# Optimization experiments

Hardware: AMD Instinct MI355X
Metric: run time of the kernel (lower is better)

Reference implementation:

```python
import jax, jax.numpy as jnp
import numpy as np

B = 16      # number of point clouds
N = 4096    # points per cloud (max segment size, static)
D = 3       # xyz


def setup_inputs() -> dict:
    key = jax.random.key(0)
    k1, k2 = jax.random.split(key)
    pred = jax.random.normal(k1, (B * N, D), dtype=jnp.float32)
    target = jax.random.normal(k2, (B * N, D), dtype=jnp.float32)
    # sorted batch assignment with equal-size segments (so N_max is static)
    batch = jnp.repeat(jnp.arange(B, dtype=jnp.int64), N)
    return {"pred": pred, "target": target, "batch": batch}


def _to_dense_batch(x, batch):
    # Faithful to torch_geometric.utils.to_dense_batch: scatter each point into
    # its (cloud, within-cloud-position) slot; padding slots stay zero.
    T = x.shape[0]
    counts = jax.ops.segment_sum(jnp.ones((T,), jnp.int32), batch, num_segments=B)
    starts = jnp.concatenate([jnp.zeros((1,), jnp.int32), jnp.cumsum(counts)[:-1]])
    pos = jnp.arange(T, dtype=jnp.int32) - starts[batch]
    dense = jnp.zeros((B, N, x.shape[1]), x.dtype).at[batch, pos].set(x)
    return dense


def _chamfer(x, y):
    # pytorch3d.loss.chamfer_distance defaults: squared L2, point_reduction="mean",
    # batch_reduction="mean"; no lengths -> padded zeros count as points (as in source).
    x2 = jnp.sum(x * x, axis=-1)                      # [B, N]
    y2 = jnp.sum(y * y, axis=-1)                      # [B, N]
    xy = jnp.einsum("bid,bjd->bij", x, y)             # [B, N, N]
    d2 = x2[:, :, None] + y2[:, None, :] - 2.0 * xy   # [B, N, N] squared dists
    cham_x = jnp.mean(jnp.min(d2, axis=2), axis=1)    # x -> nearest y, mean over points
    cham_y = jnp.mean(jnp.min(d2, axis=1), axis=1)    # y -> nearest x
    return jnp.mean(cham_x + cham_y)                  # batch mean of summed directions


def reference(pred, target, batch):
    dense_x = _to_dense_batch(pred, batch)
    dense_y = _to_dense_batch(target, batch)
    return _chamfer(dense_x, dense_y)
```

## Files before the change

kernel.cpp:

```cpp
#include <hip/hip_runtime.h>


typedef __attribute__((ext_vector_type(8))) short bf16x8;
typedef __attribute__((ext_vector_type(16))) float floatx16;

#define BB 16
#define NN 4096
#define T  256
#define NPTS (BB * NN)
#define RS 4
#define XC (4 * RS * 32)
#define NXB (NN / XC)
#define YS 2
#define YH (NN / YS)
#define YC 512
#define NC (YH / YC)
#define ONEBF 0x3F80u

__device__ __forceinline__ unsigned int f2bf(float f) {
    unsigned int u = __float_as_uint(f);
    u += 0x7fffu + ((u >> 16) & 1u);
    return u >> 16;
}
__device__ __forceinline__ float bf2f(unsigned int h) {
    return __uint_as_float(h << 16);
}

__global__ __launch_bounds__(T) void chamfer_prep(
    const float* __restrict__ pred, const float* __restrict__ target,
    uint4* __restrict__ rec0, uint4* __restrict__ rec1)
{
    int g = blockIdx.x * T + threadIdx.x;
    int set = g >> 16;
    int idx = g & (NPTS - 1);
    const float* yp = (set ? pred : target) + (size_t)idx * 3;
    float y0 = yp[0], y1 = yp[1], y2 = yp[2];
    unsigned int h0 = f2bf(y0), h1 = f2bf(y1), h2 = f2bf(y2);
    unsigned int H0 = f2bf(-2.f * bf2f(h0));
    unsigned int H1 = f2bf(-2.f * bf2f(h1));
    unsigned int H2 = f2bf(-2.f * bf2f(h2));
    unsigned int L0 = f2bf(-2.f * (y0 - bf2f(h0)));
    unsigned int L1 = f2bf(-2.f * (y1 - bf2f(h1)));
    unsigned int L2 = f2bf(-2.f * (y2 - bf2f(h2)));
    float ysq = fmaf(y0, y0, fmaf(y1, y1, y2 * y2));
    unsigned int sh = f2bf(ysq);
    unsigned int sl = f2bf(ysq - bf2f(sh));
    rec0[g] = make_uint4(H0 | (H1 << 16), H2 | (H0 << 16),
                         H1 | (H2 << 16), L0 | (L1 << 16));
    rec1[g] = make_uint4(L2 | (ONEBF << 16), ONEBF | (sh << 16),
                         sl, 0u);
}

__global__ __launch_bounds__(T, 2) void chamfer_main(
    const float* __restrict__ pred, const float* __restrict__ target,
    const uint4* __restrict__ rec0, const uint4* __restrict__ rec1,
    float* __restrict__ rowp)
{
    __shared__ uint4 ldsy[2][2][YC];

    const int xb  = blockIdx.x;
    const int b   = blockIdx.y;
    const int dir = blockIdx.z >> 1;
    const int ys  = blockIdx.z & 1;
    const float* xsrc = (dir ? target : pred) + (size_t)b * NN * 3;
    const size_t ygbase = (size_t)dir * NPTS + (size_t)b * NN + (size_t)ys * YH;
    const int tid  = threadIdx.x;
    const int lane = tid & 63, w = tid >> 6;
    const int kg   = lane >> 5, m = lane & 31;

    union U { uint4 q; bf16x8 v; };
    U au[RS];
#pragma unroll
    for (int s = 0; s < RS; ++s) {
        int xi = xb * XC + w * (RS * 32) + s * 32 + m;
        const float* xp = xsrc + (size_t)xi * 3;
        float x0 = xp[0], x1 = xp[1], x2 = xp[2];
        unsigned int h0 = f2bf(x0), h1 = f2bf(x1), h2 = f2bf(x2);
        unsigned int L0 = f2bf(x0 - bf2f(h0));
        unsigned int L1 = f2bf(x1 - bf2f(h1));
        unsigned int L2 = f2bf(x2 - bf2f(h2));
        float xsq = fmaf(x0, x0, fmaf(x1, x1, x2 * x2));
        unsigned int sh = f2bf(xsq);
        unsigned int sl = f2bf(xsq - bf2f(sh));
        au[s].q = make_uint4(kg ? (h2 | (sh << 16))    : (h0 | (h1 << 16)),
                             kg ? (sl | (ONEBF << 16)) : (h2 | (L0 << 16)),
                             kg ? ONEBF                : (L1 | (L2 << 16)),
                             kg ? 0u                   : (h0 | (h1 << 16)));
    }

    floatx16 acc[RS], zacc;
#pragma unroll
    for (int r = 0; r < 16; ++r) zacc[r] = 0.f;
#pragma unroll
    for (int s = 0; s < RS; ++s)
#pragma unroll
        for (int r = 0; r < 16; ++r) acc[s][r] = 3.402823466e38f;

    ldsy[0][0][tid]     = rec0[ygbase + tid];
    ldsy[0][0][T + tid] = rec0[ygbase + T + tid];
    ldsy[0][1][tid]     = rec1[ygbase + tid];
    ldsy[0][1][T + tid] = rec1[ygbase + T + tid];
    __syncthreads();

    for (int c = 0; c < NC; ++c) {
        const int cur = c & 1, nxt = cur ^ 1;
        uint4 s0a, s0b, s1a, s1b;
        if (c + 1 < NC) {
            size_t base = ygbase + (size_t)(c + 1) * YC;
            s0a = rec0[base + tid];
            s0b = rec0[base + T + tid];
            s1a = rec1[base + tid];
            s1b = rec1[base + T + tid];
        }
        U b0, b1;
        b0.q = ldsy[cur][kg][m];
        b1.q = ldsy[cur][kg][32 + m];
#pragma unroll 2
        for (int p = 0; p < YC / 64; ++p) {
            U n0, n1;
            int q = (p + 1) & 7;
            n0.q = ldsy[cur][kg][q * 64 + m];
            n1.q = ldsy[cur][kg][q * 64 + 32 + m];
#pragma unroll
            for (int s = 0; s < RS; ++s) {
                floatx16 d0 = __builtin_amdgcn_mfma_f32_32x32x16_bf16(
                    au[s].v, b0.v, zacc, 0, 0, 0);
                floatx16 d1 = __builtin_amdgcn_mfma_f32_32x32x16_bf16(
                    au[s].v, b1.v, zacc, 0, 0, 0);
#pragma unroll
                for (int r = 0; r < 16; ++r)
                    acc[s][r] = fminf(fminf(acc[s][r], d0[r]), d1[r]);
            }
            b0 = n0; b1 = n1;
        }
        if (c + 1 < NC) {
            ldsy[nxt][0][tid]     = s0a;
            ldsy[nxt][0][T + tid] = s0b;
            ldsy[nxt][1][tid]     = s1a;
            ldsy[nxt][1][T + tid] = s1b;
        }
        __syncthreads();
    }

    float* rp = rowp + ((size_t)((dir * BB + b) * YS + ys)) * NN + xb * XC;
#pragma unroll
    for (int s = 0; s < RS; ++s) {
#pragma unroll
        for (int r = 0; r < 16; ++r) {
            float v = acc[s][r];
            v = fminf(v, __shfl_xor(v, 1, 64));
            v = fminf(v, __shfl_xor(v, 2, 64));
            v = fminf(v, __shfl_xor(v, 4, 64));
            v = fminf(v, __shfl_xor(v, 8, 64));
            v = fminf(v, __shfl_xor(v, 16, 64));
            if (m == 0) {
                int row = (r & 3) + 8 * (r >> 2) + 4 * kg;
                rp[w * (RS * 32) + s * 32 + row] = v;
            }
        }
    }
}

__global__ __launch_bounds__(T) void chamfer_final(
    const float* __restrict__ rowp, float* __restrict__ out)
{
    float s = 0.f;
    for (int e = blockIdx.x * T + threadIdx.x; e < 2 * BB * NN;
         e += gridDim.x * T) {
        int g = e >> 12, x = e & (NN - 1);
        float v = fminf(rowp[(size_t)(2 * g) * NN + x],
                        rowp[(size_t)(2 * g + 1) * NN + x]);
        s += fmaxf(v, 0.f);
    }
#pragma unroll
    for (int off = 32; off > 0; off >>= 1)
        s += __shfl_down(s, off, 64);
    __shared__ float wsum[4];
    if ((threadIdx.x & 63) == 0) wsum[threadIdx.x >> 6] = s;
    __syncthreads();
    if (threadIdx.x == 0) {
        float t = wsum[0] + wsum[1] + wsum[2] + wsum[3];
        atomicAdd(out, t * (1.0f / (BB * NN)));
    }
}

extern "C" void kernel_launch(void* const* d_in, const int* in_sizes, int n_in,
                              void* d_out, int out_size, void* d_ws, size_t ws_size,
                              hipStream_t stream) {
    const float* pred   = (const float*)d_in[0];
    const float* target = (const float*)d_in[1];
    float* out  = (float*)d_out;
    uint4* rec0 = (uint4*)d_ws;
    uint4* rec1 = rec0 + 2 * NPTS;
    float* rowp = (float*)(rec1 + 2 * NPTS);

    hipMemsetAsync(out, 0, sizeof(float), stream);
    chamfer_prep<<<2 * NPTS / T, T, 0, stream>>>(pred, target, rec0, rec1);
    dim3 grid(NXB, BB, 2 * YS);
    chamfer_main<<<grid, T, 0, stream>>>(pred, target, rec0, rec1, rowp);
    chamfer_final<<<128, T, 0, stream>>>(rowp, out);
}
```

Measured before the change: 95.74 us.

## Halve per-wave row tiles and drop LDS double buffering for higher occupancy

Reduces rows per wave from 4 to 2 tiles, which doubles the number of x-blocks, and doubles the y chunk size so there are fewer chunk iterations. It replaces the register-staged double-buffered LDS prefetch with a single buffer loaded between two barriers, and requests 4 waves per EU instead of 2. The aim is to lower register pressure and hide latency through more resident waves rather than software pipelining. In exchange, global loads are no longer overlapped with MFMA work inside a block, and each loaded y-tile is reused across fewer x rows.

```diff
diff --git a/kernel.cpp b/kernel.cpp
--- a/kernel.cpp
+++ b/kernel.cpp
@@ -8,12 +8,12 @@
 #define NN 4096
 #define T  256
 #define NPTS (BB * NN)
-#define RS 4
+#define RS 2
 #define XC (4 * RS * 32)
 #define NXB (NN / XC)
 #define YS 2
 #define YH (NN / YS)
-#define YC 512
+#define YC 1024
 #define NC (YH / YC)
 #define ONEBF 0x3F80u
 
@@ -51,12 +51,14 @@
                          sl, 0u);
 }
 
-__global__ __launch_bounds__(T, 2) void chamfer_main(
+__global__ __launch_bounds__(T)
+__attribute__((amdgpu_waves_per_eu(4, 4)))
+void chamfer_main(
     const float* __restrict__ pred, const float* __restrict__ target,
     const uint4* __restrict__ rec0, const uint4* __restrict__ rec1,
     float* __restrict__ rowp)
 {
-    __shared__ uint4 ldsy[2][2][YC];
+    __shared__ uint4 ldsy[2][YC];
 
     const int xb  = blockIdx.x;
     const int b   = blockIdx.y;
@@ -96,50 +98,29 @@
 #pragma unroll
         for (int r = 0; r < 16; ++r) acc[s][r] = 3.402823466e38f;
 
-    ldsy[0][0][tid]     = rec0[ygbase + tid];
-    ldsy[0][0][T + tid] = rec0[ygbase + T + tid];
-    ldsy[0][1][tid]     = rec1[ygbase + tid];
-    ldsy[0][1][T + tid] = rec1[ygbase + T + tid];
-    __syncthreads();
-
     for (int c = 0; c < NC; ++c) {
-        const int cur = c & 1, nxt = cur ^ 1;
-        uint4 s0a, s0b, s1a, s1b;
-        if (c + 1 < NC) {
-            size_t base = ygbase + (size_t)(c + 1) * YC;
-            s0a = rec0[base + tid];
-            s0b = rec0[base + T + tid];
-            s1a = rec1[base + tid];
-            s1b = rec1[base + T + tid];
+        __syncthreads();
+        for (int i = tid; i < YC; i += T) {
+            ldsy[0][i] = rec0[ygbase + c * YC + i];
+            ldsy[1][i] = rec1[ygbase + c * YC + i];
         }
-        U b0, b1;
-        b0.q = ldsy[cur][kg][m];
-        b1.q = ldsy[cur][kg][32 + m];
+        __syncthreads();
 #pragma unroll 2
-        for (int p = 0; p < YC / 64; ++p) {
-            U n0, n1;
-            int q = (p + 1) & 7;
-            n0.q = ldsy[cur][kg][q * 64 + m];
-            n1.q = ldsy[cur][kg][q * 64 + 32 + m];
+        for (int t = 0; t < YC / 32; t += 2) {
+            U bu0, bu1;
+            bu0.q = ldsy[kg][t * 32 + m];
+            bu1.q = ldsy[kg][t * 32 + 32 + m];
 #pragma unroll
             for (int s = 0; s < RS; ++s) {
                 floatx16 d0 = __builtin_amdgcn_mfma_f32_32x32x16_bf16(
-                    au[s].v, b0.v, zacc, 0, 0, 0);
+                    au[s].v, bu0.v, zacc, 0, 0, 0);
                 floatx16 d1 = __builtin_amdgcn_mfma_f32_32x32x16_bf16(
-                    au[s].v, b1.v, zacc, 0, 0, 0);
+                    au[s].v, bu1.v, zacc, 0, 0, 0);
 #pragma unroll
                 for (int r = 0; r < 16; ++r)
                     acc[s][r] = fminf(fminf(acc[s][r], d0[r]), d1[r]);
             }
-            b0 = n0; b1 = n1;
         }
-        if (c + 1 < NC) {
-            ldsy[nxt][0][tid]     = s0a;
-            ldsy[nxt][0][T + tid] = s0b;
-            ldsy[nxt][1][tid]     = s1a;
-            ldsy[nxt][1][T + tid] = s1b;
-        }
-        __syncthreads();
     }
 
     float* rp = rowp + ((size_t)((dir * BB + b) * YS + ys)) * NN + xb * XC;
```

Result: slower. 125.6 us (+31.2%).
